# Kernel tuning notes

Measured on AMD Instinct MI355X. Metric: run time of the kernel, lower is better.

## Reference

```python
import jax, jax.numpy as jnp
import numpy as np

NIN, NOUT = 256, 64

def setup_inputs() -> dict:
    key = jax.random.key(0)
    k1, k2, k3, k4 = jax.random.split(key, 4)
    B, T = 4, 4096
    y = jax.random.normal(k1, (B, T, NIN), dtype=jnp.float32)
    # torch Linear(nin, nout).weight has shape [nout, nin]; store as [nin, nout]
    s = 1.0 / np.sqrt(NIN)
    Wq = jax.random.uniform(k2, (NIN, NOUT), jnp.float32, -s, s)
    Wk = jax.random.uniform(k3, (NIN, NOUT), jnp.float32, -s, s)
    Wv = jax.random.uniform(k4, (NIN, NOUT), jnp.float32, -s, s)
    return {"y": y, "Wq": Wq, "Wk": Wk, "Wv": Wv}

def reference(y, Wq, Wk, Wv):
    T = y.shape[1]
    que = y @ Wq  # [B,T,NOUT]
    key = y @ Wk
    val = y @ Wv
    att = jnp.einsum('bqd,bkd->bqk', que, key)  # [B,T,T]
    causal = jnp.tril(jnp.ones((T, T), dtype=bool))  # True = keep
    att = jnp.where(causal, att, -jnp.inf)
    att = jax.nn.softmax(att / jnp.sqrt(jnp.float32(NOUT)), axis=-1)
    return jnp.einsum('bqk,bkd->bqd', att, val)
```

## Files before the change

### kernel.cpp

```cpp
#include <hip/hip_runtime.h>
#include <hip/hip_bf16.h>

#define TLEN 4096
#define NINP 256
#define DD   64

#define QSCALE 0.18033688011112042f

typedef __attribute__((ext_vector_type(8))) short bf16x8;
typedef __attribute__((ext_vector_type(4))) float f32x4;

union U8 { bf16x8 v; uint u[4]; };

__device__ inline ushort bfu(float x) {
    union { float f; uint u; } a; a.f = x;
    uint r = a.u + 0x7fffu + ((a.u >> 16) & 1u);
    return (ushort)(r >> 16);
}
__device__ inline bf16x8 ld16(const ushort* p) {
    return *(const bf16x8*)p;
}
__device__ inline bf16x8 ld8x2(const ushort* p) {
    U8 u;
    uint2 a = *(const uint2*)p;
    uint2 b = *(const uint2*)(p + 4);
    u.u[0] = a.x; u.u[1] = a.y; u.u[2] = b.x; u.u[3] = b.y;
    return u.v;
}

__global__ __launch_bounds__(256) void prep_wt(
    const float* __restrict__ Wq, const float* __restrict__ Wk,
    const float* __restrict__ Wv, ushort* __restrict__ WT)
{
    __shared__ ushort lt[256 * 66];
    const int t = threadIdx.x;
    const int m = blockIdx.x;
    const float* W = (m == 0) ? Wq : ((m == 1) ? Wk : Wv);
    const float scale = (m == 0) ? QSCALE : 1.0f;

    #pragma unroll
    for (int j = 0; j < 16; ++j) {
        int i4 = t + 256 * j;
        float4 v = *(const float4*)&W[i4 * 4];
        int k = i4 >> 4, d = (i4 * 4) & 63;
        uint p0 = bfu(v.x * scale) | (uint(bfu(v.y * scale)) << 16);
        uint p1 = bfu(v.z * scale) | (uint(bfu(v.w * scale)) << 16);
        *(uint*)&lt[k * 66 + d]     = p0;
        *(uint*)&lt[k * 66 + d + 2] = p1;
    }
    __syncthreads();
    #pragma unroll
    for (int j = 0; j < 64; ++j) {
        int o = t + 256 * j;
        int d = o >> 8, k = o & 255;
        WT[m * 16384 + o] = lt[k * 66 + d];
    }
}

__global__ __launch_bounds__(256, 1) void qkv_kernel(
    const float* __restrict__ y, const ushort* __restrict__ WT,
    ushort* __restrict__ Qh, ushort* __restrict__ Kh, ushort* __restrict__ VhT)
{
    __shared__ ushort Wl[64 * 260];
    __shared__ ushort tb[64 * 68];

    const int t = threadIdx.x;
    const int w = t >> 6, lane = t & 63;
    const int quad = lane >> 4, l15 = lane & 15;
    const int rowbase = blockIdx.x * 64;
    const int myrow = rowbase + w * 16 + l15;

    bf16x8 afrag[8];
    const float* yrow = y + (size_t)myrow * NINP;
    #pragma unroll
    for (int s = 0; s < 8; ++s) {
        float4 lo = *(const float4*)&yrow[s * 32 + quad * 8];
        float4 hi = *(const float4*)&yrow[s * 32 + quad * 8 + 4];
        U8 u;
        u.u[0] = bfu(lo.x) | (uint(bfu(lo.y)) << 16);
        u.u[1] = bfu(lo.z) | (uint(bfu(lo.w)) << 16);
        u.u[2] = bfu(hi.x) | (uint(bfu(hi.y)) << 16);
        u.u[3] = bfu(hi.z) | (uint(bfu(hi.w)) << 16);
        afrag[s] = u.v;
    }

    f32x4 acc[3][4];
    #pragma unroll
    for (int m = 0; m < 3; ++m)
        #pragma unroll
        for (int nt = 0; nt < 4; ++nt)
            acc[m][nt] = f32x4{0.f, 0.f, 0.f, 0.f};

    for (int m = 0; m < 3; ++m) {
        __syncthreads();
        {
            int n = t >> 2, seg = t & 3;
            const ushort* src = WT + m * 16384 + n * 256 + seg * 64;
            ushort* dst = &Wl[n * 260 + seg * 64];
            #pragma unroll
            for (int j = 0; j < 16; ++j)
                ((uint2*)dst)[j] = ((const uint2*)src)[j];
        }
        __syncthreads();
        #pragma unroll
        for (int s = 0; s < 8; ++s)
            #pragma unroll
            for (int nt = 0; nt < 4; ++nt) {
                bf16x8 bfrag = ld8x2(&Wl[(nt * 16 + l15) * 260 + s * 32 + quad * 8]);
                acc[m][nt] = __builtin_amdgcn_mfma_f32_16x16x32_bf16(
                    afrag[s], bfrag, acc[m][nt], 0, 0, 0);
            }
    }

    for (int m = 0; m < 2; ++m) {
        __syncthreads();
        #pragma unroll
        for (int nt = 0; nt < 4; ++nt)
            #pragma unroll
            for (int r = 0; r < 4; ++r)
                tb[(w * 16 + quad * 4 + r) * 68 + nt * 16 + l15] = bfu(acc[m][nt][r]);
        __syncthreads();
        int row = t >> 2, seg = t & 3;
        ushort* gd = (m == 0 ? Qh : Kh) + (size_t)(rowbase + row) * DD + seg * 16;
        const ushort* sp = &tb[row * 68 + seg * 16];
        #pragma unroll
        for (int j = 0; j < 4; ++j) ((uint2*)gd)[j] = ((const uint2*)sp)[j];
    }

    __syncthreads();
    #pragma unroll
    for (int nt = 0; nt < 4; ++nt)
        #pragma unroll
        for (int r = 0; r < 4; r += 2) {
            int d = nt * 16 + l15;
            int tt = w * 16 + quad * 4 + r;
            uint pk = bfu(acc[2][nt][r]) | (uint(bfu(acc[2][nt][r + 1])) << 16);
            *(uint*)&tb[d * 68 + tt] = pk;
        }
    __syncthreads();
    {
        int d = t >> 2, seg = t & 3;
        int bb = blockIdx.x >> 6;
        int trow = (blockIdx.x & 63) * 64 + seg * 16;
        ushort* gv = VhT + ((size_t)bb * DD + d) * TLEN + trow;
        const ushort* sp = &tb[d * 68 + seg * 16];
        #pragma unroll
        for (int j = 0; j < 4; ++j) ((uint2*)gv)[j] = ((const uint2*)sp)[j];
    }
}

__global__ __launch_bounds__(256, 1) void attn_kernel(
    const ushort* __restrict__ Qh, const ushort* __restrict__ Kh,
    const ushort* __restrict__ VhT, float* __restrict__ out)
{
    __shared__ ushort Pb[4][32 * 68];
    __shared__ float  Ob[4][2048];
    __shared__ float  lb[4][32];

    const int t = threadIdx.x;
    const int w = t >> 6, lane = t & 63;
    const int quad = lane >> 4, l15 = lane & 15;
    const int b = blockIdx.x >> 6;
    const int pr = blockIdx.x & 63;

    const ushort* Qb = Qh + (size_t)b * TLEN * DD;
    const ushort* Kb = Kh + (size_t)b * TLEN * DD;
    const ushort* Vb = VhT + (size_t)b * DD * TLEN;
    float* outb = out + (size_t)b * TLEN * DD;

    for (int half = 0; half < 2; ++half) {
        const int tile = (half == 0) ? pr : (127 - pr);
        const int seg  = (half == 0) ? w : (3 - w);
        const int qb   = tile * 32;
        const int nc   = (tile + 2) >> 1;
        const int cps  = (nc + 3) >> 2;
        const int clo  = seg * cps;
        const int chi  = (nc < clo + cps) ? nc : (clo + cps);

        f32x4 o_acc[2][4];
        #pragma unroll
        for (int qt = 0; qt < 2; ++qt)
            #pragma unroll
            for (int nt = 0; nt < 4; ++nt)
                o_acc[qt][nt] = f32x4{0.f, 0.f, 0.f, 0.f};
        float l_acc[2] = {0.f, 0.f};

        if (clo < chi) {
            bf16x8 qf[2][2];
            #pragma unroll
            for (int qt = 0; qt < 2; ++qt)
                #pragma unroll
                for (int s = 0; s < 2; ++s)
                    qf[qt][s] = ld16(Qb + (size_t)(qb + qt * 16 + l15) * DD + s * 32 + quad * 8);

            bf16x8 kf[4][2];
            {
                int c0 = clo * 64;
                #pragma unroll
                for (int kt = 0; kt < 4; ++kt)
                    #pragma unroll
                    for (int s = 0; s < 2; ++s)
                        kf[kt][s] = ld16(Kb + (size_t)(c0 + kt * 16 + l15) * DD + s * 32 + quad * 8);
            }

            for (int ci = clo; ci < chi; ++ci) {
                const int c0 = ci * 64;
                bf16x8 vf[4][2];
                #pragma unroll
                for (int nt = 0; nt < 4; ++nt)
                    #pragma unroll
                    for (int s = 0; s < 2; ++s)
                        vf[nt][s] = ld16(Vb + (size_t)(nt * 16 + l15) * TLEN + c0 + s * 32 + quad * 8);

                f32x4 st[2][4];
                #pragma unroll
                for (int qt = 0; qt < 2; ++qt)
                    #pragma unroll
                    for (int kt = 0; kt < 4; ++kt)
                        st[qt][kt] = f32x4{0.f, 0.f, 0.f, 0.f};
                #pragma unroll
                for (int s = 0; s < 2; ++s)
                    #pragma unroll
                    for (int qt = 0; qt < 2; ++qt)
                        #pragma unroll
                        for (int kt = 0; kt < 4; ++kt)
                            st[qt][kt] = __builtin_amdgcn_mfma_f32_16x16x32_bf16(
                                kf[kt][s], qf[qt][s], st[qt][kt], 0, 0, 0);

                if (ci + 1 < chi) {
                    int c1 = c0 + 64;
                    #pragma unroll
                    for (int kt = 0; kt < 4; ++kt)
                        #pragma unroll
                        for (int s = 0; s < 2; ++s)
                            kf[kt][s] = ld16(Kb + (size_t)(c1 + kt * 16 + l15) * DD + s * 32 + quad * 8);
                }

                #pragma unroll
                for (int qt = 0; qt < 2; ++qt) {
                    const int q = qb + qt * 16 + l15;
                    #pragma unroll
                    for (int kt = 0; kt < 4; ++kt) {
                        const int kbase = c0 + kt * 16 + quad * 4;
                        float p[4];
                        #pragma unroll
                        for (int r = 0; r < 4; ++r) {
                            float e = exp2f(st[qt][kt][r]);
                            p[r] = (kbase + r <= q) ? e : 0.f;
                            l_acc[qt] += p[r];
                        }
                        ushort* pw = &Pb[w][(qt * 16 + l15) * 68 + kt * 16 + quad * 4];
                        *(uint*)&pw[0] = bfu(p[0]) | (uint(bfu(p[1])) << 16);
                        *(uint*)&pw[2] = bfu(p[2]) | (uint(bfu(p[3])) << 16);
                    }
                }

                #pragma unroll
                for (int qt = 0; qt < 2; ++qt) {
                    const ushort* pr_ = &Pb[w][(qt * 16 + l15) * 68];
                    bf16x8 ap0 = ld8x2(pr_ + quad * 8);
                    bf16x8 ap1 = ld8x2(pr_ + 32 + quad * 8);
                    #pragma unroll
                    for (int nt = 0; nt < 4; ++nt) {
                        o_acc[qt][nt] = __builtin_amdgcn_mfma_f32_16x16x32_bf16(
                            ap0, vf[nt][0], o_acc[qt][nt], 0, 0, 0);
                        o_acc[qt][nt] = __builtin_amdgcn_mfma_f32_16x16x32_bf16(
                            ap1, vf[nt][1], o_acc[qt][nt], 0, 0, 0);
                    }
                }
            }

            #pragma unroll
            for (int qt = 0; qt < 2; ++qt) {
                l_acc[qt] += __shfl_xor(l_acc[qt], 16, 64);
                l_acc[qt] += __shfl_xor(l_acc[qt], 32, 64);
            }
        }

        #pragma unroll
        for (int qt = 0; qt < 2; ++qt) {
            #pragma unroll
            for (int nt = 0; nt < 4; ++nt)
                #pragma unroll
                for (int r = 0; r < 4; ++r)
                    Ob[w][(qt * 16 + quad * 4 + r) * 64 + nt * 16 + l15] = o_acc[qt][nt][r];
            if (quad == 0) lb[w][qt * 16 + l15] = l_acc[qt];
        }
        __syncthreads();

        #pragma unroll
        for (int e = 0; e < 8; ++e) {
            int idx = t + 256 * e;
            int q = idx >> 6;
            float s = Ob[0][idx] + Ob[1][idx] + Ob[2][idx] + Ob[3][idx];
            float ls = lb[0][q] + lb[1][q] + lb[2][q] + lb[3][q];
            outb[(size_t)(qb + q) * DD + (idx & 63)] = s * __builtin_amdgcn_rcpf(ls);
        }
        __syncthreads();
    }
}

extern "C" void kernel_launch(void* const* d_in, const int* in_sizes, int n_in,
                              void* d_out, int out_size, void* d_ws, size_t ws_size,
                              hipStream_t stream) {
    const float* y  = (const float*)d_in[0];
    const float* Wq = (const float*)d_in[1];
    const float* Wk = (const float*)d_in[2];
    const float* Wv = (const float*)d_in[3];
    float* outp = (float*)d_out;

    const int rows = in_sizes[0] / NINP;
    const int nb = rows / TLEN;

    ushort* WT  = (ushort*)d_ws;
    ushort* Qh  = WT + 3 * 16384;
    ushort* Kh  = Qh + (size_t)rows * DD;
    ushort* VhT = Kh + (size_t)rows * DD;

    prep_wt<<<3, 256, 0, stream>>>(Wq, Wk, Wv, WT);
    qkv_kernel<<<rows / 64, 256, 0, stream>>>(y, WT, Qh, Kh, VhT);
    attn_kernel<<<nb * 64, 256, 0, stream>>>(Qh, Kh, VhT, outp);
}
```

Before: 114.1 us.

## Split attention across 8 waves, shrink QKV tiles, parallelize weight prep, skip masking

The attention kernel moves from 4 to 8 waves per block, so each query tile's key chunks are spread over more waves. Causal masking now runs only on the last chunk, bf16 packing uses a perm-based round instead of the full round-to-nearest-even, and the final reduction is vectorized. The QKV projection uses 32-row blocks with a 2x2 wave split, giving twice as many blocks and a higher occupancy hint, and weight prep is spread across 48 blocks with no LDS transpose. Trade-offs: more LDS per attention block, a slightly different bf16 rounding, and the masking condition relies on the last chunk being the only diagonal one.

```diff
diff --git a/kernel.cpp b/kernel.cpp
--- a/kernel.cpp
+++ b/kernel.cpp
@@ -11,11 +11,16 @@
 typedef __attribute__((ext_vector_type(4))) float f32x4;
 
 union U8 { bf16x8 v; uint u[4]; };
+union F32U { float f; uint u; };
 
 __device__ inline ushort bfu(float x) {
-    union { float f; uint u; } a; a.f = x;
+    F32U a; a.f = x;
     uint r = a.u + 0x7fffu + ((a.u >> 16) & 1u);
     return (ushort)(r >> 16);
+}
+__device__ inline uint pk2(float p0, float p1) {
+    F32U a, b; a.f = p0; b.f = p1;
+    return __builtin_amdgcn_perm(b.u + 0x8000u, a.u + 0x8000u, 0x07060302u);
 }
 __device__ inline bf16x8 ld16(const ushort* p) {
     return *(const bf16x8*)p;
@@ -32,43 +37,31 @@
     const float* __restrict__ Wq, const float* __restrict__ Wk,
     const float* __restrict__ Wv, ushort* __restrict__ WT)
 {
-    __shared__ ushort lt[256 * 66];
     const int t = threadIdx.x;
-    const int m = blockIdx.x;
+    const int m = blockIdx.x >> 4;
+    const int d0 = (blockIdx.x & 15) * 4;
     const float* W = (m == 0) ? Wq : ((m == 1) ? Wk : Wv);
     const float scale = (m == 0) ? QSCALE : 1.0f;
-
-    #pragma unroll
-    for (int j = 0; j < 16; ++j) {
-        int i4 = t + 256 * j;
-        float4 v = *(const float4*)&W[i4 * 4];
-        int k = i4 >> 4, d = (i4 * 4) & 63;
-        uint p0 = bfu(v.x * scale) | (uint(bfu(v.y * scale)) << 16);
-        uint p1 = bfu(v.z * scale) | (uint(bfu(v.w * scale)) << 16);
-        *(uint*)&lt[k * 66 + d]     = p0;
-        *(uint*)&lt[k * 66 + d + 2] = p1;
-    }
-    __syncthreads();
-    #pragma unroll
-    for (int j = 0; j < 64; ++j) {
-        int o = t + 256 * j;
-        int d = o >> 8, k = o & 255;
-        WT[m * 16384 + o] = lt[k * 66 + d];
-    }
-}
-
-__global__ __launch_bounds__(256, 1) void qkv_kernel(
+    float4 v = *(const float4*)&W[t * DD + d0];
+    WT[m * 16384 + (d0 + 0) * 256 + t] = bfu(v.x * scale);
+    WT[m * 16384 + (d0 + 1) * 256 + t] = bfu(v.y * scale);
+    WT[m * 16384 + (d0 + 2) * 256 + t] = bfu(v.z * scale);
+    WT[m * 16384 + (d0 + 3) * 256 + t] = bfu(v.w * scale);
+}
+
+__global__ __launch_bounds__(256, 2) void qkv_kernel(
     const float* __restrict__ y, const ushort* __restrict__ WT,
     ushort* __restrict__ Qh, ushort* __restrict__ Kh, ushort* __restrict__ VhT)
 {
     __shared__ ushort Wl[64 * 260];
-    __shared__ ushort tb[64 * 68];
+    __shared__ ushort tb[2304];
 
     const int t = threadIdx.x;
     const int w = t >> 6, lane = t & 63;
     const int quad = lane >> 4, l15 = lane & 15;
-    const int rowbase = blockIdx.x * 64;
-    const int myrow = rowbase + w * 16 + l15;
+    const int rgrp = w & 1, ngrp = w >> 1;
+    const int rowbase = blockIdx.x * 32;
+    const int myrow = rowbase + rgrp * 16 + l15;
 
     bf16x8 afrag[8];
     const float* yrow = y + (size_t)myrow * NINP;
@@ -84,12 +77,12 @@
         afrag[s] = u.v;
     }
 
-    f32x4 acc[3][4];
+    f32x4 acc[3][2];
     #pragma unroll
     for (int m = 0; m < 3; ++m)
         #pragma unroll
-        for (int nt = 0; nt < 4; ++nt)
-            acc[m][nt] = f32x4{0.f, 0.f, 0.f, 0.f};
+        for (int nj = 0; nj < 2; ++nj)
+            acc[m][nj] = f32x4{0.f, 0.f, 0.f, 0.f};
 
     for (int m = 0; m < 3; ++m) {
         __syncthreads();
@@ -105,57 +98,85 @@
         #pragma unroll
         for (int s = 0; s < 8; ++s)
             #pragma unroll
-            for (int nt = 0; nt < 4; ++nt) {
+            for (int nj = 0; nj < 2; ++nj) {
+                int nt = ngrp * 2 + nj;
                 bf16x8 bfrag = ld8x2(&Wl[(nt * 16 + l15) * 260 + s * 32 + quad * 8]);
-                acc[m][nt] = __builtin_amdgcn_mfma_f32_16x16x32_bf16(
-                    afrag[s], bfrag, acc[m][nt], 0, 0, 0);
+                acc[m][nj] = __builtin_amdgcn_mfma_f32_16x16x32_bf16(
+                    afrag[s], bfrag, acc[m][nj], 0, 0, 0);
             }
     }
 
     for (int m = 0; m < 2; ++m) {
         __syncthreads();
         #pragma unroll
-        for (int nt = 0; nt < 4; ++nt)
+        for (int nj = 0; nj < 2; ++nj) {
+            int nt = ngrp * 2 + nj;
             #pragma unroll
             for (int r = 0; r < 4; ++r)
-                tb[(w * 16 + quad * 4 + r) * 68 + nt * 16 + l15] = bfu(acc[m][nt][r]);
-        __syncthreads();
-        int row = t >> 2, seg = t & 3;
-        ushort* gd = (m == 0 ? Qh : Kh) + (size_t)(rowbase + row) * DD + seg * 16;
-        const ushort* sp = &tb[row * 68 + seg * 16];
-        #pragma unroll
-        for (int j = 0; j < 4; ++j) ((uint2*)gd)[j] = ((const uint2*)sp)[j];
+                tb[(rgrp * 16 + quad * 4 + r) * 68 + nt * 16 + l15] = bfu(acc[m][nj][r]);
+        }
+        __syncthreads();
+        int row = t >> 3, c0 = (t & 7) * 8;
+        ushort* gd = (m == 0 ? Qh : Kh) + (size_t)(rowbase + row) * DD + c0;
+        const ushort* sp = &tb[row * 68 + c0];
+        ((uint2*)gd)[0] = ((const uint2*)sp)[0];
+        ((uint2*)gd)[1] = ((const uint2*)sp)[1];
     }
 
     __syncthreads();
     #pragma unroll
-    for (int nt = 0; nt < 4; ++nt)
+    for (int nj = 0; nj < 2; ++nj) {
+        int nt = ngrp * 2 + nj;
+        int d = nt * 16 + l15;
         #pragma unroll
         for (int r = 0; r < 4; r += 2) {
-            int d = nt * 16 + l15;
-            int tt = w * 16 + quad * 4 + r;
-            uint pk = bfu(acc[2][nt][r]) | (uint(bfu(acc[2][nt][r + 1])) << 16);
-            *(uint*)&tb[d * 68 + tt] = pk;
-        }
+            int tt = rgrp * 16 + quad * 4 + r;
+            *(uint*)&tb[d * 36 + tt] = pk2(acc[2][nj][r], acc[2][nj][r + 1]);
+        }
+    }
     __syncthreads();
     {
         int d = t >> 2, seg = t & 3;
-        int bb = blockIdx.x >> 6;
-        int trow = (blockIdx.x & 63) * 64 + seg * 16;
-        ushort* gv = VhT + ((size_t)bb * DD + d) * TLEN + trow;
-        const ushort* sp = &tb[d * 68 + seg * 16];
-        #pragma unroll
-        for (int j = 0; j < 4; ++j) ((uint2*)gv)[j] = ((const uint2*)sp)[j];
-    }
-}
-
-__global__ __launch_bounds__(256, 1) void attn_kernel(
+        int bb = blockIdx.x >> 7;
+        int tofs = (blockIdx.x & 127) * 32 + seg * 8;
+        ushort* gv = VhT + ((size_t)bb * DD + d) * TLEN + tofs;
+        const ushort* sp = &tb[d * 36 + seg * 8];
+        ((uint2*)gv)[0] = ((const uint2*)sp)[0];
+        ((uint2*)gv)[1] = ((const uint2*)sp)[1];
+    }
+}
+
+template <bool MASK>
+__device__ inline void softmax_store(
+    f32x4 st[2][4], ushort* Pw, int qb, int c0, int l15, int quad, float* l_acc)
+{
+    #pragma unroll
+    for (int qt = 0; qt < 2; ++qt) {
+        const int q = qb + qt * 16 + l15;
+        #pragma unroll
+        for (int kt = 0; kt < 4; ++kt) {
+            const int kbase = c0 + kt * 16 + quad * 4;
+            float p[4];
+            #pragma unroll
+            for (int r = 0; r < 4; ++r) {
+                float e = exp2f(st[qt][kt][r]);
+                p[r] = (!MASK || (kbase + r <= q)) ? e : 0.f;
+                l_acc[qt] += p[r];
+            }
+            ushort* pw = Pw + (qt * 16 + l15) * 68 + kt * 16 + quad * 4;
+            *(uint*)&pw[0] = pk2(p[0], p[1]);
+            *(uint*)&pw[2] = pk2(p[2], p[3]);
+        }
+    }
+}
+
+__global__ __launch_bounds__(512, 2) void attn_kernel(
     const ushort* __restrict__ Qh, const ushort* __restrict__ Kh,
     const ushort* __restrict__ VhT, float* __restrict__ out)
 {
-    __shared__ ushort Pb[4][32 * 68];
-    __shared__ float  Ob[4][2048];
-    __shared__ float  lb[4][32];
+    __shared__ ushort Pb[8][32 * 68];
+    __shared__ float  Ob[8][2048];
+    __shared__ float  lb[8][32];
 
     const int t = threadIdx.x;
     const int w = t >> 6, lane = t & 63;
@@ -170,10 +191,10 @@
 
     for (int half = 0; half < 2; ++half) {
         const int tile = (half == 0) ? pr : (127 - pr);
-        const int seg  = (half == 0) ? w : (3 - w);
+        const int seg  = (half == 0) ? w : (7 - w);
         const int qb   = tile * 32;
         const int nc   = (tile + 2) >> 1;
-        const int cps  = (nc + 3) >> 2;
+        const int cps  = (nc + 7) >> 3;
         const int clo  = seg * cps;
         const int chi  = (nc < clo + cps) ? nc : (clo + cps);
 
@@ -236,24 +257,10 @@
                             kf[kt][s] = ld16(Kb + (size_t)(c1 + kt * 16 + l15) * DD + s * 32 + quad * 8);
                 }
 
-                #pragma unroll
-                for (int qt = 0; qt < 2; ++qt) {
-                    const int q = qb + qt * 16 + l15;
-                    #pragma unroll
-                    for (int kt = 0; kt < 4; ++kt) {
-                        const int kbase = c0 + kt * 16 + quad * 4;
-                        float p[4];
-                        #pragma unroll
-                        for (int r = 0; r < 4; ++r) {
-                            float e = exp2f(st[qt][kt][r]);
-                            p[r] = (kbase + r <= q) ? e : 0.f;
-                            l_acc[qt] += p[r];
-                        }
-                        ushort* pw = &Pb[w][(qt * 16 + l15) * 68 + kt * 16 + quad * 4];
-                        *(uint*)&pw[0] = bfu(p[0]) | (uint(bfu(p[1])) << 16);
-                        *(uint*)&pw[2] = bfu(p[2]) | (uint(bfu(p[3])) << 16);
-                    }
-                }
+                if (ci == nc - 1)
+                    softmax_store<true>(st, Pb[w], qb, c0, l15, quad, l_acc);
+                else
+                    softmax_store<false>(st, Pb[w], qb, c0, l15, quad, l_acc);
 
                 #pragma unroll
                 for (int qt = 0; qt < 2; ++qt) {
@@ -288,13 +295,19 @@
         }
         __syncthreads();
 
-        #pragma unroll
-        for (int e = 0; e < 8; ++e) {
-            int idx = t + 256 * e;
-            int q = idx >> 6;
-            float s = Ob[0][idx] + Ob[1][idx] + Ob[2][idx] + Ob[3][idx];
-            float ls = lb[0][q] + lb[1][q] + lb[2][q] + lb[3][q];
-            outb[(size_t)(qb + q) * DD + (idx & 63)] = s * __builtin_amdgcn_rcpf(ls);
+        {
+            int q = t >> 4, d0 = (t & 15) * 4;
+            f32x4 s = f32x4{0.f, 0.f, 0.f, 0.f};
+            float ls = 0.f;
+            #pragma unroll
+            for (int ww = 0; ww < 8; ++ww) {
+                s += *(const f32x4*)&Ob[ww][q * 64 + d0];
+                ls += lb[ww][q];
+            }
+            float inv = __builtin_amdgcn_rcpf(ls);
+            float4 r;
+            r.x = s[0] * inv; r.y = s[1] * inv; r.z = s[2] * inv; r.w = s[3] * inv;
+            *(float4*)&outb[(size_t)(qb + q) * DD + d0] = r;
         }
         __syncthreads();
     }
@@ -317,7 +330,7 @@
     ushort* Kh  = Qh + (size_t)rows * DD;
     ushort* VhT = Kh + (size_t)rows * DD;
 
-    prep_wt<<<3, 256, 0, stream>>>(Wq, Wk, Wv, WT);
-    qkv_kernel<<<rows / 64, 256, 0, stream>>>(y, WT, Qh, Kh, VhT);
-    attn_kernel<<<nb * 64, 256, 0, stream>>>(Qh, Kh, VhT, outp);
-}
+    prep_wt<<<48, 256, 0, stream>>>(Wq, Wk, Wv, WT);
+    qkv_kernel<<<rows / 32, 256, 0, stream>>>(y, WT, Qh, Kh, VhT);
+    attn_kernel<<<nb * 64, 512, 0, stream>>>(Qh, Kh, VhT, outp);
+}
```

New measurement: 116.5 us. 2.1% more time.
